# Kernel tuning notes

Hardware: AMD Instinct MI355X
Metric: run time of the kernel (lower is better)

## Reference

```python
import jax, jax.numpy as jnp
import numpy as np
import math

D_MODEL = 1024
D_STATE = 16
D_CONV = 4
DT_RANK = math.ceil(D_MODEL / 16)  # 64


def setup_inputs() -> dict:
    key = jax.random.key(0)
    ks = jax.random.split(key, 10)
    B, L, D, N, R = 2, 4096, D_MODEL, D_STATE, DT_RANK
    x = jax.random.normal(ks[0], (B, L, D), dtype=jnp.float32)
    # A = arange(1, N+1) repeated over D; A_log = log(A)
    A_log = jnp.log(jnp.tile(jnp.arange(1, N + 1, dtype=jnp.float32), (D, 1)))  # (D, N)
    D_param = jnp.ones((D,), dtype=jnp.float32)
    # projection weights (torch Linear convention: W @ x, W shape (out, in))
    W_dt1 = jax.random.normal(ks[1], (R, D), dtype=jnp.float32) / np.sqrt(D)   # x_proj_dt
    W_dt2 = jax.random.normal(ks[2], (D, R), dtype=jnp.float32) / np.sqrt(R)   # dt_proj weight
    # dt bias init as in _init_dt_bias
    dt0 = jnp.exp(jax.random.uniform(ks[3], (D,)) * (math.log(0.1) - math.log(0.001)) + math.log(0.001))
    b_dt = dt0 + jnp.log(-jnp.expm1(-dt0))
    W_B = jax.random.normal(ks[4], (N, D), dtype=jnp.float32) / np.sqrt(D)
    W_C = jax.random.normal(ks[5], (N, D), dtype=jnp.float32) / np.sqrt(D)
    conv_w = jax.random.normal(ks[6], (D, 1, D_CONV), dtype=jnp.float32) / np.sqrt(D_CONV)  # depthwise (O,I/g,K)
    conv_b = jax.random.normal(ks[7], (D,), dtype=jnp.float32) * 0.01
    return {"x": x, "A_log": A_log, "D_param": D_param, "W_dt1": W_dt1,
            "W_dt2": W_dt2, "b_dt": b_dt, "W_B": W_B, "W_C": W_C,
            "conv_w": conv_w, "conv_b": conv_b}


def _forward(x, A_log, D_param, W_dt1, W_dt2, b_dt, W_B, W_C, conv_w, conv_b):
    B, L, D = x.shape
    N = A_log.shape[1]
    # depthwise causal conv: torch pads both sides by d_conv-1 then slices [:L]
    # == left pad (d_conv-1), right pad 0
    xc = jax.lax.conv_general_dilated(
        jnp.swapaxes(x, 1, 2),  # (B, D, L)
        conv_w,                  # (D, 1, K)
        window_strides=(1,), padding=[(D_CONV - 1, 0)],
        dimension_numbers=("NCH", "OIH", "NCH"),
        feature_group_count=D)
    x_conv = jax.nn.silu(jnp.swapaxes(xc, 1, 2) + conv_b)  # (B, L, D)

    dt = jax.nn.softplus(jnp.einsum("bld,rd->blr", x_conv, W_dt1) @ W_dt2.T + b_dt)  # (B,L,D)
    B_ssm = jnp.einsum("bld,nd->bln", x_conv, W_B)  # (B,L,N)
    C_ssm = jnp.einsum("bld,nd->bln", x_conv, W_C)  # (B,L,N)
    A = -jnp.exp(A_log)  # (D, N)

    def step(h, inputs):
        x_t, dt_t, B_t, C_t = inputs  # (B,D),(B,D),(B,N),(B,N)
        dtA = jnp.clip(dt_t[..., None] * A[None], -10.0, 0.0)
        A_bar = jnp.clip(jnp.exp(dtA), 0.0, 0.999)               # (B,D,N)
        B_bar = jnp.clip(jnp.clip(dt_t, 0.0, 1.0)[..., None] * B_t[:, None, :], -10.0, 10.0)
        h = jnp.clip(A_bar * h + B_bar * x_t[..., None], -100.0, 100.0)
        y_t = jnp.clip(jnp.einsum("bdn,bn->bd", h, C_t) + D_param * x_t, -50.0, 50.0)
        return h, y_t

    h0 = jnp.zeros((B, D, N), dtype=x.dtype)
    xs = (jnp.swapaxes(x_conv, 0, 1), jnp.swapaxes(dt, 0, 1),
          jnp.swapaxes(B_ssm, 0, 1), jnp.swapaxes(C_ssm, 0, 1))  # leading axis L
    _, y = jax.lax.scan(step, h0, xs)  # y: (L, B, D)
    return jnp.swapaxes(y, 0, 1)


def reference(x, A_log, D_param, W_dt1, W_dt2, b_dt, W_B, W_C, conv_w, conv_b):
    return _forward(x, A_log, D_param, W_dt1, W_dt2, b_dt, W_B, W_C, conv_w, conv_b)
```

## Files before the change

kernel.cpp:

```cpp
#include <hip/hip_runtime.h>
#include <hip/hip_bf16.h>

#define BB 2
#define LL 4096
#define DD 1024
#define NN 16
#define RR 64
#define KK 4
#define ROWS 8

#define T_CH 32
#define NCH (LL / T_CH)


__device__ __forceinline__ float med3f(float x, float lo, float hi) {
    return __builtin_amdgcn_fmed3f(x, lo, hi);
}

template<int CTRL>
__device__ __forceinline__ float dpp_ror(float v) {
    int r = __builtin_amdgcn_update_dpp(0, __builtin_bit_cast(int, v), CTRL, 0xf, 0xf, true);
    return __builtin_bit_cast(float, r);
}

__device__ __forceinline__ float silu_f(float z) {
    float e = __expf(-z);
    return z * __builtin_amdgcn_rcpf(1.0f + e);
}

__device__ __forceinline__ float softplus_f(float z) {
    float e = __expf(-fabsf(z));
    return fmaxf(z, 0.0f) + __logf(1.0f + e);
}

__global__ __launch_bounds__(256) void prep_kernel(
    const float* __restrict__ Wdt1, const float* __restrict__ Wdt2,
    const float* __restrict__ WB, const float* __restrict__ WC,
    float* __restrict__ Wdt1T, float* __restrict__ Wdt2T, float* __restrict__ WBCT)
{
    int i = blockIdx.x * 256 + threadIdx.x;
    if (i < 65536) {
        int k = i >> 6, r = i & 63;
        Wdt1T[i] = Wdt1[r * 1024 + k];
    }
    if (i < 65536) {
        int r = i >> 10, d = i & 1023;
        Wdt2T[i] = Wdt2[d * 64 + r];
    }
    if (i < 32768) {
        int k = i >> 5, o = i & 31;
        WBCT[i] = (o < 16) ? WB[o * 1024 + k] : WC[(o - 16) * 1024 + k];
    }
}

__global__ __launch_bounds__(256) void proj_kernel(
    const float* __restrict__ x,
    const float* __restrict__ conv_w, const float* __restrict__ conv_b,
    const float* __restrict__ Wdt1T, const float* __restrict__ Wdt2T,
    const float* __restrict__ b_dt, const float* __restrict__ WBCT,
    float2* __restrict__ xdtT, float2* __restrict__ bcT)
{
    __shared__ alignas(16) float xc8[1024 * ROWS];
    __shared__ alignas(16) float part[2048];
    __shared__ alignas(16) float dtpre[64 * ROWS];

    const int t = threadIdx.x;
    const int blk = blockIdx.x;
    const int b = blk >> 9;
    const int l0 = (blk & 511) << 3;
    const int ch = l0 >> 5;
    const int tt0 = l0 & 31;
    const float* xb = x + (size_t)b * LL * DD;

    float xc_reg[4][ROWS];
    #pragma unroll
    for (int dd = 0; dd < 4; ++dd) {
        int d = t + dd * 256;
        float4 w4 = reinterpret_cast<const float4*>(conv_w)[d];
        float cb = conv_b[d];
        float xv[ROWS + 3];
        #pragma unroll
        for (int j = 0; j < ROWS + 3; ++j) {
            int l = l0 - 3 + j;
            xv[j] = (l >= 0) ? xb[(size_t)l * DD + d] : 0.0f;
        }
        #pragma unroll
        for (int r = 0; r < ROWS; ++r) {
            float s = cb + xv[r] * w4.x + xv[r + 1] * w4.y + xv[r + 2] * w4.z + xv[r + 3] * w4.w;
            float v = silu_f(s);
            xc_reg[dd][r] = v;
        }
        float4 lo = make_float4(xc_reg[dd][0], xc_reg[dd][1], xc_reg[dd][2], xc_reg[dd][3]);
        float4 hi = make_float4(xc_reg[dd][4], xc_reg[dd][5], xc_reg[dd][6], xc_reg[dd][7]);
        reinterpret_cast<float4*>(&xc8[d * ROWS])[0] = lo;
        reinterpret_cast<float4*>(&xc8[d * ROWS])[1] = hi;
    }
    __syncthreads();

    const float4* xr4 = reinterpret_cast<const float4*>(xc8);

    {
        int r = t & 63, seg = t >> 6;
        float acc[ROWS];
        #pragma unroll
        for (int q = 0; q < ROWS; ++q) acc[q] = 0.0f;
        const float* wp = Wdt1T + (size_t)(seg * 256) * 64 + r;
        int kbase = seg * 256;
        for (int i = 0; i < 256; ++i) {
            float wv = wp[(size_t)i * 64];
            float4 a = xr4[(kbase + i) * 2];
            float4 c = xr4[(kbase + i) * 2 + 1];
            acc[0] += a.x * wv; acc[1] += a.y * wv; acc[2] += a.z * wv; acc[3] += a.w * wv;
            acc[4] += c.x * wv; acc[5] += c.y * wv; acc[6] += c.z * wv; acc[7] += c.w * wv;
        }
        #pragma unroll
        for (int q = 0; q < ROWS; ++q) part[seg * 512 + r * 8 + q] = acc[q];
    }
    __syncthreads();
    {
        int idx = t;
        #pragma unroll
        for (int rep = 0; rep < 2; ++rep, idx += 256) {
            float s = part[idx] + part[512 + idx] + part[1024 + idx] + part[1536 + idx];
            dtpre[idx] = s;
        }
    }
    __syncthreads();

    const float4* dp4 = reinterpret_cast<const float4*>(dtpre);
    float2* xTbase = xdtT + (((size_t)b * NCH + ch) * DD) * T_CH;
    #pragma unroll
    for (int dd = 0; dd < 4; ++dd) {
        int d = t + dd * 256;
        float bd = b_dt[d];
        float acc[ROWS];
        #pragma unroll
        for (int q = 0; q < ROWS; ++q) acc[q] = bd;
        const float* wp = Wdt2T + d;
        for (int r = 0; r < 64; ++r) {
            float wv = wp[(size_t)r * 1024];
            float4 p0 = dp4[r * 2];
            float4 p1 = dp4[r * 2 + 1];
            acc[0] += p0.x * wv; acc[1] += p0.y * wv; acc[2] += p0.z * wv; acc[3] += p0.w * wv;
            acc[4] += p1.x * wv; acc[5] += p1.y * wv; acc[6] += p1.z * wv; acc[7] += p1.w * wv;
        }
        float sp[ROWS];
        #pragma unroll
        for (int row = 0; row < ROWS; ++row) sp[row] = softplus_f(acc[row]);
        float4* dst4 = (float4*)(xTbase + (size_t)d * T_CH + tt0);
        #pragma unroll
        for (int q = 0; q < 4; ++q)
            dst4[q] = make_float4(xc_reg[dd][2 * q], sp[2 * q],
                                  xc_reg[dd][2 * q + 1], sp[2 * q + 1]);
    }

    {
        int o = t & 31, seg = t >> 5;
        float acc[ROWS];
        #pragma unroll
        for (int q = 0; q < ROWS; ++q) acc[q] = 0.0f;
        const float* wp = WBCT + (size_t)(seg * 128) * 32 + o;
        int kbase = seg * 128;
        for (int i = 0; i < 128; ++i) {
            float wv = wp[(size_t)i * 32];
            float4 a = xr4[(kbase + i) * 2];
            float4 c = xr4[(kbase + i) * 2 + 1];
            acc[0] += a.x * wv; acc[1] += a.y * wv; acc[2] += a.z * wv; acc[3] += a.w * wv;
            acc[4] += c.x * wv; acc[5] += c.y * wv; acc[6] += c.z * wv; acc[7] += c.w * wv;
        }
        #pragma unroll
        for (int q = 0; q < ROWS; ++q) part[seg * 256 + o * 8 + q] = acc[q];
    }
    __syncthreads();
    if (t < 128) {
        int n2 = t >> 3, row = t & 7;
        float Bv = 0.0f, Cv = 0.0f;
        #pragma unroll
        for (int seg = 0; seg < 8; ++seg) {
            Bv += part[seg * 256 + n2 * 8 + row];
            Cv += part[seg * 256 + (n2 + 16) * 8 + row];
        }
        bcT[(((size_t)b * NCH + ch) * NN + n2) * T_CH + tt0 + row] = make_float2(Bv, Cv);
    }
}

__device__ __forceinline__ void chunk_load(const float4* __restrict__ xp4,
                                           const float4* __restrict__ bp4,
                                           float4 (&X)[16], float4 (&Bc)[16])
{
    #pragma unroll
    for (int j = 0; j < 16; ++j) X[j] = xp4[j];
    #pragma unroll
    for (int j = 0; j < 16; ++j) Bc[j] = bp4[j];
}

__device__ __forceinline__ void chunk_compute(
    const float4 (&X)[16], const float4 (&Bc)[16],
    float& h, float A2, float Dp, int n, float* __restrict__ yc)
{
    float yr0 = 0.0f, yr1 = 0.0f;
    #pragma unroll
    for (int t = 0; t < T_CH; ++t) {
        const int j = t >> 1, hf = t & 1;
        float xv = hf ? X[j].z : X[j].x;
        float dt = hf ? X[j].w : X[j].y;
        float Bv = hf ? Bc[j].z : Bc[j].x;
        float Cv = hf ? Bc[j].w : Bc[j].y;
        float dtA = fmaxf(dt * A2, -14.426950408889634f);
        float Abar = fminf(exp2f(dtA), 0.999f);
        float tt = med3f(fminf(dt, 1.0f) * Bv, -10.0f, 10.0f);
        h = med3f(fmaf(Abar, h, tt * xv), -100.0f, 100.0f);
        float p = h * Cv;
        p += dpp_ror<0x121>(p);
        p += dpp_ror<0x122>(p);
        p += dpp_ror<0x124>(p);
        p += dpp_ror<0x128>(p);
        float yv = med3f(fmaf(Dp, xv, p), -50.0f, 50.0f);
        const int ts = t & 15;
        if (t < 16) yr0 = (n == ts) ? yv : yr0;
        else        yr1 = (n == ts) ? yv : yr1;
    }
    yc[(size_t)n * DD] = yr0;
    yc[(size_t)(16 + n) * DD] = yr1;
}

__global__ __launch_bounds__(64, 1) void scan_kernel(
    const float2* __restrict__ xdtT, const float2* __restrict__ bcT,
    const float* __restrict__ A_log, const float* __restrict__ Dparam,
    float* __restrict__ y)
{
    const int w = blockIdx.x;
    const int b = w >> 8;
    const int dbase = (w & 255) << 2;
    const int lane = threadIdx.x;
    const int n = lane & 15;
    const int dl = lane >> 4;
    const int d = dbase + dl;

    const float A2 = -__expf(A_log[d * NN + n]) * 1.4426950408889634f;
    const float Dp = Dparam[d];

    const float4* xp = (const float4*)(xdtT + ((size_t)b * NCH * DD + d) * T_CH);
    const float4* bp = (const float4*)(bcT + ((size_t)b * NCH * NN + n) * T_CH);
    const size_t XSTR = (size_t)DD * T_CH / 2;
    const size_t BSTR = (size_t)NN * T_CH / 2;

    float* yb = y + (size_t)b * LL * DD + dbase + dl;

    float4 XA[16], BA[16], XB[16], BB2[16];
    float h = 0.0f;

    chunk_load(xp, bp, XA, BA);
    chunk_load(xp + XSTR, bp + BSTR, XB, BB2);
    asm volatile("s_waitcnt vmcnt(32)" ::: "memory");
    chunk_compute(XA, BA, h, A2, Dp, n, yb);

    #pragma unroll 1
    for (int c = 2; c <= NCH - 2; c += 2) {
        chunk_load(xp + (size_t)c * XSTR, bp + (size_t)c * BSTR, XA, BA);
        asm volatile("s_waitcnt vmcnt(34)" ::: "memory");
        chunk_compute(XB, BB2, h, A2, Dp, n, yb + (size_t)(c - 1) * T_CH * DD);
        chunk_load(xp + (size_t)(c + 1) * XSTR, bp + (size_t)(c + 1) * BSTR, XB, BB2);
        asm volatile("s_waitcnt vmcnt(34)" ::: "memory");
        chunk_compute(XA, BA, h, A2, Dp, n, yb + (size_t)c * T_CH * DD);
    }

    asm volatile("s_waitcnt vmcnt(2)" ::: "memory");
    chunk_compute(XB, BB2, h, A2, Dp, n, yb + (size_t)(NCH - 1) * T_CH * DD);
}

extern "C" void kernel_launch(void* const* d_in, const int* in_sizes, int n_in,
                              void* d_out, int out_size, void* d_ws, size_t ws_size,
                              hipStream_t stream) {
    const float* x      = (const float*)d_in[0];
    const float* A_log  = (const float*)d_in[1];
    const float* Dparam = (const float*)d_in[2];
    const float* W_dt1  = (const float*)d_in[3];
    const float* W_dt2  = (const float*)d_in[4];
    const float* b_dt   = (const float*)d_in[5];
    const float* W_B    = (const float*)d_in[6];
    const float* W_C    = (const float*)d_in[7];
    const float* conv_w = (const float*)d_in[8];
    const float* conv_b = (const float*)d_in[9];
    float* y = (float*)d_out;

    float* ws = (float*)d_ws;
    float2* xdtT = (float2*)ws;
    float2* bcT  = (float2*)(ws + (size_t)2 * BB * LL * DD);
    float* Wdt1T = ws + (size_t)2 * BB * LL * DD + (size_t)2 * BB * LL * NN;
    float* Wdt2T = Wdt1T + 65536;
    float* WBCT  = Wdt2T + 65536;

    prep_kernel<<<256, 256, 0, stream>>>(W_dt1, W_dt2, W_B, W_C, Wdt1T, Wdt2T, WBCT);
    proj_kernel<<<BB * (LL / ROWS), 256, 0, stream>>>(x, conv_w, conv_b, Wdt1T, Wdt2T,
                                                      b_dt, WBCT, xdtT, bcT);
    scan_kernel<<<BB * (DD / 4), 64, 0, stream>>>(xdtT, bcT, A_log, Dparam, y);
}
```

Baseline: 491.9 us.

## Restructure scan into 8-step granules with a four-deep load ring

Changes the intermediate layout from 32-step chunks to 8-step granules. The scan kernel now keeps a ring of four granule buffers, prefetching three granules ahead with explicit vmcnt waits instead of double-buffering 32-step chunks. Per-step exp, B-scaling and D*x terms are computed in a batch before the serial recurrence, which shortens the dependent chain. The smaller register footprint and deeper, finer-grained prefetch aim to hide memory latency better. The risks are more, smaller loads and reliance on hand-tuned waitcnt counts.

Result: faster. 454.9 us (-7.5%).

```diff
diff --git a/kernel.cpp b/kernel.cpp
--- a/kernel.cpp
+++ b/kernel.cpp
@@ -9,8 +9,8 @@
 #define KK 4
 #define ROWS 8
 
-#define T_CH 32
-#define NCH (LL / T_CH)
+#define TG 8
+#define NG (LL / TG)
 
 
 __device__ __forceinline__ float med3f(float x, float lo, float hi) {
@@ -68,8 +68,7 @@
     const int blk = blockIdx.x;
     const int b = blk >> 9;
     const int l0 = (blk & 511) << 3;
-    const int ch = l0 >> 5;
-    const int tt0 = l0 & 31;
+    const int gg = l0 >> 3;
     const float* xb = x + (size_t)b * LL * DD;
 
     float xc_reg[4][ROWS];
@@ -87,8 +86,7 @@
         #pragma unroll
         for (int r = 0; r < ROWS; ++r) {
             float s = cb + xv[r] * w4.x + xv[r + 1] * w4.y + xv[r + 2] * w4.z + xv[r + 3] * w4.w;
-            float v = silu_f(s);
-            xc_reg[dd][r] = v;
+            xc_reg[dd][r] = silu_f(s);
         }
         float4 lo = make_float4(xc_reg[dd][0], xc_reg[dd][1], xc_reg[dd][2], xc_reg[dd][3]);
         float4 hi = make_float4(xc_reg[dd][4], xc_reg[dd][5], xc_reg[dd][6], xc_reg[dd][7]);
@@ -128,7 +126,7 @@
     __syncthreads();
 
     const float4* dp4 = reinterpret_cast<const float4*>(dtpre);
-    float2* xTbase = xdtT + (((size_t)b * NCH + ch) * DD) * T_CH;
+    float2* xTbase = xdtT + ((size_t)b * NG + gg) * DD * TG;
     #pragma unroll
     for (int dd = 0; dd < 4; ++dd) {
         int d = t + dd * 256;
@@ -147,7 +145,7 @@
         float sp[ROWS];
         #pragma unroll
         for (int row = 0; row < ROWS; ++row) sp[row] = softplus_f(acc[row]);
-        float4* dst4 = (float4*)(xTbase + (size_t)d * T_CH + tt0);
+        float4* dst4 = (float4*)(xTbase + (size_t)d * TG);
         #pragma unroll
         for (int q = 0; q < 4; ++q)
             dst4[q] = make_float4(xc_reg[dd][2 * q], sp[2 * q],
@@ -180,49 +178,53 @@
             Bv += part[seg * 256 + n2 * 8 + row];
             Cv += part[seg * 256 + (n2 + 16) * 8 + row];
         }
-        bcT[(((size_t)b * NCH + ch) * NN + n2) * T_CH + tt0 + row] = make_float2(Bv, Cv);
-    }
-}
-
-__device__ __forceinline__ void chunk_load(const float4* __restrict__ xp4,
-                                           const float4* __restrict__ bp4,
-                                           float4 (&X)[16], float4 (&Bc)[16])
-{
-    #pragma unroll
-    for (int j = 0; j < 16; ++j) X[j] = xp4[j];
-    #pragma unroll
-    for (int j = 0; j < 16; ++j) Bc[j] = bp4[j];
-}
-
-__device__ __forceinline__ void chunk_compute(
-    const float4 (&X)[16], const float4 (&Bc)[16],
-    float& h, float A2, float Dp, int n, float* __restrict__ yc)
-{
-    float yr0 = 0.0f, yr1 = 0.0f;
-    #pragma unroll
-    for (int t = 0; t < T_CH; ++t) {
-        const int j = t >> 1, hf = t & 1;
-        float xv = hf ? X[j].z : X[j].x;
-        float dt = hf ? X[j].w : X[j].y;
-        float Bv = hf ? Bc[j].z : Bc[j].x;
-        float Cv = hf ? Bc[j].w : Bc[j].y;
-        float dtA = fmaxf(dt * A2, -14.426950408889634f);
-        float Abar = fminf(exp2f(dtA), 0.999f);
-        float tt = med3f(fminf(dt, 1.0f) * Bv, -10.0f, 10.0f);
-        h = med3f(fmaf(Abar, h, tt * xv), -100.0f, 100.0f);
+        bcT[(((size_t)b * NG + gg) * NN + n2) * TG + row] = make_float2(Bv, Cv);
+    }
+}
+
+struct Gran { float4 X[4]; float4 B[4]; };
+
+__device__ __forceinline__ void gload(Gran& G, const float4* __restrict__ xq,
+                                      const float4* __restrict__ bq) {
+    #pragma unroll
+    for (int j = 0; j < 4; ++j) G.X[j] = xq[j];
+    #pragma unroll
+    for (int j = 0; j < 4; ++j) G.B[j] = bq[j];
+}
+
+template<int PAR>
+__device__ __forceinline__ void consume(const Gran& G, float& h, float& yr,
+                                        float A2, float Dp, int n) {
+    float a[TG], u[TG], Dx[TG];
+    #pragma unroll
+    for (int t = 0; t < TG; ++t) {
+        const int j = t >> 1; const bool hf = t & 1;
+        float xv = hf ? G.X[j].z : G.X[j].x;
+        float dt = hf ? G.X[j].w : G.X[j].y;
+        a[t] = fminf(__builtin_amdgcn_exp2f(fmaxf(dt * A2, -14.426950408889634f)), 0.999f);
+        u[t] = med3f(fminf(dt, 1.0f) * (hf ? G.B[j].z : G.B[j].x), -10.0f, 10.0f) * xv;
+        Dx[t] = Dp * xv;
+    }
+    #pragma unroll
+    for (int t = 0; t < TG; ++t) {
+        const int j = t >> 1; const bool hf = t & 1;
+        float Cv = hf ? G.B[j].w : G.B[j].y;
+        h = med3f(fmaf(a[t], h, u[t]), -100.0f, 100.0f);
         float p = h * Cv;
         p += dpp_ror<0x121>(p);
         p += dpp_ror<0x122>(p);
         p += dpp_ror<0x124>(p);
         p += dpp_ror<0x128>(p);
-        float yv = med3f(fmaf(Dp, xv, p), -50.0f, 50.0f);
-        const int ts = t & 15;
-        if (t < 16) yr0 = (n == ts) ? yv : yr0;
-        else        yr1 = (n == ts) ? yv : yr1;
-    }
-    yc[(size_t)n * DD] = yr0;
-    yc[(size_t)(16 + n) * DD] = yr1;
-}
+        float yv = med3f(p + Dx[t], -50.0f, 50.0f);
+        yr = (n == PAR * TG + t) ? yv : yr;
+    }
+}
+
+#define SCAN_ITER(RING, PAR, DO_STORE, LG)                                 \
+    asm volatile("s_waitcnt vmcnt(24)" ::: "memory");                      \
+    consume<PAR>(RING, h, yr, A2, Dp, n);                                  \
+    if (DO_STORE) { *yq = yr; yq += 16 * DD; }                             \
+    gload(RING, xq + (size_t)(LG) * 4096, bq + (size_t)(LG) * 64);
 
 __global__ __launch_bounds__(64, 1) void scan_kernel(
     const float2* __restrict__ xdtT, const float2* __restrict__ bcT,
@@ -240,33 +242,37 @@
     const float A2 = -__expf(A_log[d * NN + n]) * 1.4426950408889634f;
     const float Dp = Dparam[d];
 
-    const float4* xp = (const float4*)(xdtT + ((size_t)b * NCH * DD + d) * T_CH);
-    const float4* bp = (const float4*)(bcT + ((size_t)b * NCH * NN + n) * T_CH);
-    const size_t XSTR = (size_t)DD * T_CH / 2;
-    const size_t BSTR = (size_t)NN * T_CH / 2;
-
-    float* yb = y + (size_t)b * LL * DD + dbase + dl;
-
-    float4 XA[16], BA[16], XB[16], BB2[16];
-    float h = 0.0f;
-
-    chunk_load(xp, bp, XA, BA);
-    chunk_load(xp + XSTR, bp + BSTR, XB, BB2);
-    asm volatile("s_waitcnt vmcnt(32)" ::: "memory");
-    chunk_compute(XA, BA, h, A2, Dp, n, yb);
+    const float4* xq = (const float4*)(xdtT + ((size_t)b * NG * DD + d) * TG);
+    const float4* bq = (const float4*)(bcT + ((size_t)b * NG * NN + n) * TG);
+    float* yq = y + ((size_t)b * LL + n) * DD + dbase + dl;
+
+    Gran r0, r1, r2, r3;
+    float h = 0.0f, yr = 0.0f;
+
+    gload(r0, xq, bq);
+    gload(r1, xq + 4096, bq + 64);
+    gload(r2, xq + 2 * 4096, bq + 2 * 64);
+    gload(r3, xq + 3 * 4096, bq + 3 * 64);
 
     #pragma unroll 1
-    for (int c = 2; c <= NCH - 2; c += 2) {
-        chunk_load(xp + (size_t)c * XSTR, bp + (size_t)c * BSTR, XA, BA);
-        asm volatile("s_waitcnt vmcnt(34)" ::: "memory");
-        chunk_compute(XB, BB2, h, A2, Dp, n, yb + (size_t)(c - 1) * T_CH * DD);
-        chunk_load(xp + (size_t)(c + 1) * XSTR, bp + (size_t)(c + 1) * BSTR, XB, BB2);
-        asm volatile("s_waitcnt vmcnt(34)" ::: "memory");
-        chunk_compute(XA, BA, h, A2, Dp, n, yb + (size_t)c * T_CH * DD);
-    }
-
-    asm volatile("s_waitcnt vmcnt(2)" ::: "memory");
-    chunk_compute(XB, BB2, h, A2, Dp, n, yb + (size_t)(NCH - 1) * T_CH * DD);
+    for (int blk = 0; blk < 127; ++blk) {
+        const int g4 = blk * 4;
+        SCAN_ITER(r0, 0, false, g4 + 4)
+        SCAN_ITER(r1, 1, true,  g4 + 5)
+        SCAN_ITER(r2, 0, false, g4 + 6)
+        SCAN_ITER(r3, 1, true,  g4 + 7)
+    }
+
+    asm volatile("s_waitcnt vmcnt(24)" ::: "memory");
+    consume<0>(r0, h, yr, A2, Dp, n);
+    asm volatile("s_waitcnt vmcnt(16)" ::: "memory");
+    consume<1>(r1, h, yr, A2, Dp, n);
+    *yq = yr; yq += 16 * DD;
+    asm volatile("s_waitcnt vmcnt(8)" ::: "memory");
+    consume<0>(r2, h, yr, A2, Dp, n);
+    asm volatile("s_waitcnt vmcnt(0)" ::: "memory");
+    consume<1>(r3, h, yr, A2, Dp, n);
+    *yq = yr;
 }
 
 extern "C" void kernel_launch(void* const* d_in, const int* in_sizes, int n_in,
```
